# Kernel tuning notes

Measured on AMD Instinct MI355X. Metric: run time of the kernel, lower is better.

The kernel has to match this reference:

```python
import jax, jax.numpy as jnp
import numpy as np

V, E, H, HC = 20000, 300, 512, 256
B, N, LE, NW, LW, NC, LC = 16, 64, 16, 8, 16, 64, 16


def _gru_dir(xg, W_hh, b_hh, reverse):
    # xg: [B, T, 3*Hc] precomputed input gates; returns final hidden [B, Hc]
    xs = jnp.swapaxes(xg, 0, 1)
    if reverse:
        xs = xs[::-1]
    h0 = jnp.zeros((xg.shape[0], W_hh.shape[1]), xg.dtype)

    def step(h, xt):
        hr, hz, hn = jnp.split(h @ W_hh.T + b_hh, 3, axis=-1)
        xr, xz, xn = jnp.split(xt, 3, axis=-1)
        r = jax.nn.sigmoid(xr + hr)
        z = jax.nn.sigmoid(xz + hz)
        n = jnp.tanh(xn + r * hn)
        return (1.0 - z) * n + z * h, None

    hT, _ = jax.lax.scan(step, h0, xs)
    return hT


def _bigru(x, Wif, Whf, bif, bhf, Wib, Whb, bib, bhb):
    # x: [B, T, D] -> concat(fwd final, bwd final) = [B, 2*Hc]  (matches torch h_n.permute(1,0,2).reshape)
    hf = _gru_dir(x @ Wif.T + bif, Whf, bhf, False)
    hb = _gru_dir(x @ Wib.T + bib, Whb, bhb, True)
    return jnp.concatenate([hf, hb], axis=-1)


def setup_inputs() -> dict:
    key = jax.random.key(0)
    ks = iter(jax.random.split(key, 64))
    f = lambda *s: jax.random.normal(next(ks), s, jnp.float32) * 0.05
    ri = lambda *s: jax.random.randint(next(ks), s, 0, V)
    return {
        "emb_table": f(V, E),
        "W_prj": f(H, E),
        "dn_Wif": f(3 * HC, H), "dn_Whf": f(3 * HC, HC), "dn_bif": f(3 * HC), "dn_bhf": f(3 * HC),
        "dn_Wib": f(3 * HC, H), "dn_Whb": f(3 * HC, HC), "dn_bib": f(3 * HC), "dn_bhb": f(3 * HC),
        "W_e": f(H, H), "W_l": f(H, H), "W_w": f(H, H),
        "Wg": f(H, H), "bg": f(H),
        "diff_Wif": f(3 * H, H), "diff_Whf": f(3 * H, H), "diff_bif": f(3 * H), "diff_bhf": f(3 * H),
        "diff_Wib": f(3 * H, H), "diff_Whb": f(3 * H, H), "diff_bib": f(3 * H), "diff_bhb": f(3 * H),
        "Wc": f(1, 2 * H), "bc": f(1),
        "Wa1": f(2 * H, 2 * H), "ba1": f(2 * H), "Wa2": f(1, 2 * H), "ba2": f(1),
        "local_adj": jnp.zeros((64, 64), jnp.float32),
        "obs": ri(B, 32),
        "local_graph": ri(64, 8),
        "entities": ri(B, N, LE),
        "locals_": ri(B, N, LE),
        "worlds": ri(B, N, NW, LW),
        "commands": ri(B, NC, LC),
    }


def reference(emb_table, W_prj,
              dn_Wif, dn_Whf, dn_bif, dn_bhf, dn_Wib, dn_Whb, dn_bib, dn_bhb,
              W_e, W_l, W_w, Wg, bg,
              diff_Wif, diff_Whf, diff_bif, diff_bhf, diff_Wib, diff_Whb, diff_bib, diff_bhb,
              Wc, bc, Wa1, ba1, Wa2, ba2,
              local_adj, obs, local_graph, entities, locals_, worlds, commands):
    dn = (dn_Wif, dn_Whf, dn_bif, dn_bhf, dn_Wib, dn_Whb, dn_bib, dn_bhb)
    emb = lambda ids: emb_table[ids] @ W_prj.T  # embedding lookup + no-bias projection to H

    b, n, le = entities.shape
    ent_h = _bigru(emb(entities).reshape(b * n, le, H), *dn).reshape(b, n, H)
    ll = locals_.shape[-1]
    loc_h = _bigru(emb(locals_).reshape(b * n, ll, H), *dn).reshape(b, n, H)
    nw, lw = worlds.shape[2], worlds.shape[3]
    w_h = _bigru(emb(worlds).reshape(b * n * nw, lw, H), *dn).reshape(b, n, nw, H)
    worlds_sum = (w_h @ W_w).sum(axis=2)  # [b, n, H]

    # torch.ones(H,H) + W_e  ==  broadcastable 1.0 + W_e
    graph_hidden = jax.nn.elu(ent_h @ (1.0 + W_e)) + jax.nn.elu(loc_h @ W_l) + worlds_sum
    graph_encoding = jax.nn.elu(jax.nn.elu(graph_hidden) @ Wg.T + bg)  # graph_prj (dropout=eval identity)

    # value network: 'diff' path
    diff_h = _bigru(graph_encoding, diff_Wif, diff_Whf, diff_bif, diff_bhf,
                    diff_Wib, diff_Whb, diff_bib, diff_bhb)  # [b, 2H]
    value = (diff_h @ Wc.T + bc).reshape(b, 1, 1)

    nc, lc = commands.shape[1], commands.shape[2]
    c_h = _bigru(emb(commands).reshape(b * nc, lc, H), *dn).reshape(b, nc, H)

    rep = jnp.concatenate([
        jnp.broadcast_to(c_h[:, None, :, :], (b, n, nc, H)),
        jnp.broadcast_to(graph_encoding[:, :, None, :], (b, n, nc, H)),
    ], axis=-1)  # [b, n, nc, 2H]
    s = jax.nn.elu(rep @ Wa1.T + ba1) @ Wa2.T + ba2  # att_cmd (dropout p=0)
    scores = s[..., 0].mean(axis=1)  # mean over entities -> [b, nc]

    mask = commands.sum(axis=2) > 0
    probs = jax.nn.softmax(jnp.where(mask, scores, -1e9), axis=1)
    index = jnp.argmax(probs, axis=1).reshape(1, b, 1)  # deterministic stand-in for multinomial(1)
    return scores, index, value
```

## Files before the change

### kernel.cpp

```cpp
#include <hip/hip_runtime.h>
#include <stdint.h>

#define DEVFN __device__ __forceinline__

typedef __attribute__((ext_vector_type(4))) float fx4;
typedef __attribute__((ext_vector_type(8))) short sx8;
typedef __bf16 bf16x8 __attribute__((ext_vector_type(8)));

DEVFN float eluf(float x){ return x>0.f ? x : __expf(x)-1.f; }
DEVFN float sigm(float x){ return 1.f/(1.f+__expf(-x)); }
DEVFN float tanhf_(float x){ float cx=fminf(10.f,fmaxf(-10.f,x)); float e=__expf(-2.f*cx); return (1.f-e)/(1.f+e); }

DEVFN fx4 MFMA(sx8 a, sx8 b, fx4 c){
  return __builtin_amdgcn_mfma_f32_16x16x32_bf16(
      __builtin_bit_cast(bf16x8,a), __builtin_bit_cast(bf16x8,b), c, 0,0,0);
}
DEVFN void splitf(float x, short& hi, short& lo){
  __bf16 h = (__bf16)x; hi = __builtin_bit_cast(short, h);
  __bf16 l = (__bf16)(x - (float)h); lo = __builtin_bit_cast(short, l);
}

struct TT { const float* src; float* dst; int srows, scols, drows; };
struct TTs { TT t[4]; };
__global__ void k_prep_t(TTs ts){
  TT tk = ts.t[blockIdx.y];
  size_t tot = (size_t)tk.drows * tk.srows;
  for (size_t i = (size_t)blockIdx.x*256 + threadIdx.x; i < tot; i += (size_t)gridDim.x*256){
    int c = (int)(i / tk.srows), r = (int)(i % tk.srows);
    tk.dst[i] = (c < tk.scols) ? tk.src[(size_t)r*tk.scols + c] : 0.f;
  }
}
struct PL { const float* src; __bf16* hi; __bf16* lo; size_t n; };
struct PLs { PL t[2]; };
__global__ void k_prep_planes(PLs ts){
  PL tk = ts.t[blockIdx.y];
  for (size_t i = (size_t)blockIdx.x*256 + threadIdx.x; i < tk.n; i += (size_t)gridDim.x*256){
    float x = tk.src[i];
    __bf16 h = (__bf16)x;
    tk.hi[i] = h; tk.lo[i] = (__bf16)(x - (float)h);
  }
}
struct BC { const float* src; __bf16* dst; size_t n; };
struct BCs { BC t[2]; };
__global__ void k_prep_b16(BCs ts){
  BC tk = ts.t[blockIdx.y];
  for (size_t i = (size_t)blockIdx.x*256 + threadIdx.x; i < tk.n; i += (size_t)gridDim.x*256)
    tk.dst[i] = (__bf16)tk.src[i];
}
__global__ void k_toks(const int* __restrict__ ents, const int* __restrict__ locs,
                       const int* __restrict__ wrl, const int* __restrict__ cmd,
                       int* __restrict__ toks){
  int idx = blockIdx.x*256 + threadIdx.x;
  if (idx >= 2*16*11264) return;
  int dir = idx / (16*11264);
  int rem = idx % (16*11264);
  int s = rem / 11264, c = rem % 11264;
  const int* tp;
  if (c<1024) tp = ents + c*16;
  else if (c<2048) tp = locs + (c-1024)*16;
  else if (c<10240) tp = wrl + (c-2048)*16;
  else tp = cmd + (c-10240)*16;
  toks[idx] = tp[dir ? 15-s : s];
}
__global__ void k_cat_bias(const float* __restrict__ a, const float* __restrict__ b,
                           float* __restrict__ o){
  int i = blockIdx.x*256 + threadIdx.x;
  if (i < 768) o[i] = a[i];
  else if (i < 1536) o[i] = b[i-768];
}

template<int EPI, int OBF>
__global__ __launch_bounds__(256) void gemm_k(
    const float* __restrict__ A, const float* __restrict__ B,
    const float* __restrict__ bias, void* __restrict__ out,
    int M, int N, int Kpad, int Kreal, int lda, int ldb)
{
  int bm = blockIdx.y*64, bn = blockIdx.x*64;
  int tid = threadIdx.x, l = tid&63, w = tid>>6;
  int wm = (w>>1)*32, wn = (w&1)*32;
  int lr = l&15, lk = l>>4;
  fx4 acc[2][2] = {};
  for (int k0 = 0; k0 < Kpad; k0 += 32) {
    sx8 ahi[2], alo[2], bhi[2], blo[2];
    bool full = (k0 + 32 <= Kreal);
    #pragma unroll
    for (int i=0;i<2;i++){
      int row = bm + wm + i*16 + lr; row = row < M ? row : M-1;
      int col = bn + wn + i*16 + lr;
      const float* ap = A + (size_t)row*lda + k0 + lk*8;
      const float* bp = B + (size_t)col*ldb + k0 + lk*8;
      float av[8], bv[8];
      if (full){
        *(fx4*)av = *(const fx4*)ap; *(fx4*)(av+4) = *(const fx4*)(ap+4);
        *(fx4*)bv = *(const fx4*)bp; *(fx4*)(bv+4) = *(const fx4*)(bp+4);
      } else {
        #pragma unroll
        for (int j=0;j<8;j++){
          int k = k0 + lk*8 + j;
          av[j] = (k < Kreal) ? ap[j] : 0.f;
          bv[j] = (k < Kreal) ? bp[j] : 0.f;
        }
      }
      #pragma unroll
      for (int j=0;j<8;j++){
        short h,lo2; splitf(av[j], h, lo2); ahi[i][j]=h; alo[i][j]=lo2;
        splitf(bv[j], h, lo2); bhi[i][j]=h; blo[i][j]=lo2;
      }
    }
    #pragma unroll
    for (int i=0;i<2;i++)
      #pragma unroll
      for (int j=0;j<2;j++){
        acc[i][j] = MFMA(alo[i], bhi[j], acc[i][j]);
        acc[i][j] = MFMA(ahi[i], blo[j], acc[i][j]);
        acc[i][j] = MFMA(ahi[i], bhi[j], acc[i][j]);
      }
  }
  #pragma unroll
  for (int i=0;i<2;i++)
    #pragma unroll
    for (int j=0;j<2;j++)
      #pragma unroll
      for (int q=0;q<4;q++){
        int m = bm + wm + i*16 + lk*4 + q;
        int n = bn + wn + j*16 + lr;
        if (m < M){
          float v = acc[i][j][q];
          if (EPI>=1) v += bias[n];
          if (EPI==2) v = eluf(v);
          if (OBF) ((__bf16*)out)[(size_t)m*N + n] = (__bf16)v;
          else     ((float*)out)[(size_t)m*N + n] = v;
        }
      }
}

__global__ __launch_bounds__(256) void dn_step(
  const __bf16* __restrict__ Hshi, const __bf16* __restrict__ Hslo,
  __bf16* __restrict__ Hdhi, __bf16* __restrict__ Hdlo,
  const __bf16* __restrict__ Whi, const __bf16* __restrict__ Wlo,
  const float* __restrict__ bias, const float* __restrict__ T, int tstride,
  const int* __restrict__ toks,
  float* __restrict__ seqh, int s, int dir)
{
  int bm = blockIdx.x*64;
  int bj = blockIdx.y*64;
  int tid = threadIdx.x, l = tid&63, w = tid>>6;
  int wm = (w>>1)*32, wn = (w&1)*32;
  int lr = l&15, lk = l>>4;
  fx4 acc[2][2][3] = {};
  if (s > 0){
    for (int kk=0;kk<8;kk++){
      sx8 ah[2], al[2];
      #pragma unroll
      for (int i=0;i<2;i++){
        int m = bm + wm + i*16 + lr;
        ah[i] = *(const sx8*)(Hshi + (size_t)m*256 + kk*32 + lk*8);
        al[i] = *(const sx8*)(Hslo + (size_t)m*256 + kk*32 + lk*8);
      }
      #pragma unroll
      for (int jt=0;jt<2;jt++){
        #pragma unroll
        for (int role=0;role<3;role++){
          int col = role*256 + bj + wn + jt*16 + lr;
          sx8 bhf = *(const sx8*)(Whi + (size_t)col*256 + kk*32 + lk*8);
          sx8 blf = *(const sx8*)(Wlo + (size_t)col*256 + kk*32 + lk*8);
          #pragma unroll
          for (int i=0;i<2;i++){
            fx4 a = acc[i][jt][role];
            a = MFMA(al[i], bhf, a);
            a = MFMA(ah[i], blf, a);
            a = MFMA(ah[i], bhf, a);
            acc[i][jt][role] = a;
          }
        }
      }
    }
  }
  const int* tks = toks + s*11264;
  #pragma unroll
  for (int i=0;i<2;i++){
    #pragma unroll
    for (int q=0;q<4;q++){
      int m = bm + wm + i*16 + lk*4 + q;
      int tok = tks[m];
      const float* trow = T + (size_t)tok*tstride;
      #pragma unroll
      for (int jt=0;jt<2;jt++){
        int j = bj + wn + jt*16 + lr;
        float hr = acc[i][jt][0][q] + bias[j];
        float hz = acc[i][jt][1][q] + bias[256+j];
        float hn = acc[i][jt][2][q] + bias[512+j];
        float xr = trow[j], xz = trow[256+j], xn = trow[512+j];
        float ho = 0.f;
        if (s > 0) ho = (float)Hshi[(size_t)m*256+j] + (float)Hslo[(size_t)m*256+j];
        float r = sigm(xr+hr), z = sigm(xz+hz);
        float n = tanhf_(xn + r*hn);
        float v = (1.f-z)*n + z*ho;
        __bf16 hh = (__bf16)v;
        Hdhi[(size_t)m*256+j] = hh;
        Hdlo[(size_t)m*256+j] = (__bf16)(v - (float)hh);
        if (s == 15) seqh[(size_t)m*512 + dir*256 + j] = v;
      }
    }
  }
}

__global__ void k_wsum(const float* __restrict__ seqh, float* __restrict__ ws){
  int r = blockIdx.x;
  for (int c = threadIdx.x; c < 512; c += 256){
    float a = 0.f;
    #pragma unroll
    for (int w8=0; w8<8; w8++) a += seqh[((size_t)2048 + r*8 + w8)*512 + c];
    ws[(size_t)r*512 + c] = a;
  }
}
__global__ void k_rowsum(const float* __restrict__ seqh, float* __restrict__ rs){
  int r = blockIdx.x, l = threadIdx.x;
  float a = 0.f;
  for (int c=l;c<512;c+=64) a += seqh[(size_t)r*512+c];
  #pragma unroll
  for (int o=32;o>0;o>>=1) a += __shfl_down(a,o);
  if (l==0) rs[r]=a;
}
__global__ void k_combine(const float* __restrict__ E1, const float* __restrict__ E2,
                          const float* __restrict__ E3, const float* __restrict__ rs,
                          float* __restrict__ y){
  size_t i = (size_t)blockIdx.x*256 + threadIdx.x;
  int r = (int)(i >> 9);
  float g = eluf(E1[i] + rs[r]) + eluf(E2[i]) + E3[i];
  y[i] = eluf(g);
}

__global__ __launch_bounds__(256) void diff_step(
  const float* __restrict__ hsrc, float* __restrict__ hdst,
  const __bf16* __restrict__ Whf, const __bf16* __restrict__ Whb,
  const float* __restrict__ bhf, const float* __restrict__ bhb,
  const __bf16* __restrict__ Xf, const __bf16* __restrict__ Xb, int t)
{
  int wg = blockIdx.x;
  int dir = wg>>3, seg = wg&7;
  const __bf16* W = dir? Whb: Whf;
  const float* bh = dir? bhb: bhf;
  const __bf16* X = dir? Xb: Xf;
  int tt = dir? 63-t : t;
  int tid = threadIdx.x, l = tid&63, w = tid>>6;
  int lr=l&15, lk=l>>4;
  int jbase = seg*64 + w*16;
  fx4 acc[3] = {};
  const float* hrow = hsrc + (size_t)dir*16*512;
  for (int kk=0;kk<16;kk++){
    const float* ap = hrow + (size_t)lr*512 + kk*32 + lk*8;
    float av[8];
    *(fx4*)av = *(const fx4*)ap; *(fx4*)(av+4) = *(const fx4*)(ap+4);
    sx8 ah, al;
    #pragma unroll
    for (int j=0;j<8;j++){ short h,lo; splitf(av[j],h,lo); ah[j]=h; al[j]=lo; }
    #pragma unroll
    for (int role=0;role<3;role++){
      int col = role*512 + jbase + lr;
      sx8 b = *(const sx8*)(W + (size_t)col*512 + kk*32 + lk*8);
      acc[role] = MFMA(al, b, acc[role]);
      acc[role] = MFMA(ah, b, acc[role]);
    }
  }
  #pragma unroll
  for (int q=0;q<4;q++){
    int m = lk*4+q;
    int j = jbase + lr;
    float hr = acc[0][q] + bh[j];
    float hz = acc[1][q] + bh[512+j];
    float hn = acc[2][q] + bh[1024+j];
    const __bf16* xrow = X + ((size_t)m*64 + tt)*1536;
    float xr = (float)xrow[j], xz = (float)xrow[512+j], xn = (float)xrow[1024+j];
    float ho = hrow[(size_t)m*512 + j];
    float r = sigm(xr+hr), z = sigm(xz+hz);
    float n = tanhf_(xn + r*hn);
    hdst[((size_t)dir*16 + m)*512 + j] = (1.f-z)*n + z*ho;
  }
}

__global__ __launch_bounds__(256) void k_score(
  const float* __restrict__ Amat, const float* __restrict__ Gmat,
  const float* __restrict__ Wa2, const float* __restrict__ ba2, float* __restrict__ sc)
{
  __shared__ float red[4];
  int p = blockIdx.x, b = p>>6, tid = threadIdx.x;
  float av[4], wv[4];
  #pragma unroll
  for (int k=0;k<4;k++){ av[k] = Amat[(size_t)p*1024 + tid + k*256]; wv[k] = Wa2[tid + k*256]; }
  float acc = 0.f;
  for (int n=0;n<64;n++){
    const float* g = Gmat + ((size_t)b*64+n)*1024;
    #pragma unroll
    for (int k=0;k<4;k++) acc += wv[k]*eluf(av[k] + g[tid + k*256]);
  }
  #pragma unroll
  for (int o=32;o>0;o>>=1) acc += __shfl_down(acc,o);
  if ((tid&63)==0) red[tid>>6] = acc;
  __syncthreads();
  if (tid==0) sc[p] = (red[0]+red[1]+red[2]+red[3])*(1.f/64.f) + ba2[0];
}

__global__ void k_final(const float* __restrict__ sc, const int* __restrict__ cmds,
                        const float* __restrict__ hfin, const float* __restrict__ Wc,
                        const float* __restrict__ bc, float* __restrict__ out)
{
  int b = blockIdx.x, l = threadIdx.x;
  out[b*64+l] = sc[b*64+l];
  int ssum = 0;
  const int* cr = cmds + (b*64+l)*16;
  #pragma unroll
  for (int k=0;k<16;k++) ssum += cr[k];
  float v = ssum>0 ? sc[b*64+l] : -1e9f;
  int idx = l;
  #pragma unroll
  for (int o=32;o>0;o>>=1){
    float ov = __shfl_down(v,o); int oi = __shfl_down(idx,o);
    if (ov > v || (ov==v && oi<idx)) { v=ov; idx=oi; }
  }
  if (l==0) out[1024 + b] = (float)idx;
  float a = 0.f;
  for (int j=l;j<512;j+=64) a += hfin[(size_t)b*512+j] * Wc[j];
  for (int j=l;j<512;j+=64) a += hfin[(size_t)(16+b)*512+j] * Wc[512+j];
  #pragma unroll
  for (int o=32;o>0;o>>=1) a += __shfl_down(a,o);
  if (l==0) out[1040 + b] = a + bc[0];
}

static inline void launch_gemm(hipStream_t st, const float* A, const float* B,
                               const float* bias, void* out, int M, int N,
                               int Kpad, int Kreal, int lda, int ldb, int epi, int obf)
{
  dim3 g(N/64, (M+63)/64), blk(256);
  if      (epi==0 && obf==0) gemm_k<0,0><<<g,blk,0,st>>>(A,B,bias,out,M,N,Kpad,Kreal,lda,ldb);
  else if (epi==1 && obf==0) gemm_k<1,0><<<g,blk,0,st>>>(A,B,bias,out,M,N,Kpad,Kreal,lda,ldb);
  else if (epi==2 && obf==0) gemm_k<2,0><<<g,blk,0,st>>>(A,B,bias,out,M,N,Kpad,Kreal,lda,ldb);
  else                       gemm_k<1,1><<<g,blk,0,st>>>(A,B,bias,out,M,N,Kpad,Kreal,lda,ldb);
}

extern "C" void kernel_launch(void* const* d_in, const int* in_sizes, int n_in,
                              void* d_out, int out_size, void* d_ws, size_t ws_size,
                              hipStream_t stream) {
  (void)in_sizes; (void)n_in; (void)out_size;
  const float* emb   = (const float*)d_in[0];
  const float* W_prj = (const float*)d_in[1];
  const float* dnWif = (const float*)d_in[2];
  const float* dnWhf = (const float*)d_in[3];
  const float* dnbif = (const float*)d_in[4];
  const float* dnbhf = (const float*)d_in[5];
  const float* dnWib = (const float*)d_in[6];
  const float* dnWhb = (const float*)d_in[7];
  const float* dnbib = (const float*)d_in[8];
  const float* dnbhb = (const float*)d_in[9];
  const float* W_e   = (const float*)d_in[10];
  const float* W_l   = (const float*)d_in[11];
  const float* W_w   = (const float*)d_in[12];
  const float* Wg    = (const float*)d_in[13];
  const float* bg    = (const float*)d_in[14];
  const float* dWif  = (const float*)d_in[15];
  const float* dWhf  = (const float*)d_in[16];
  const float* dbif  = (const float*)d_in[17];
  const float* dbhf  = (const float*)d_in[18];
  const float* dWib  = (const float*)d_in[19];
  const float* dWhb  = (const float*)d_in[20];
  const float* dbib  = (const float*)d_in[21];
  const float* dbhb  = (const float*)d_in[22];
  const float* Wc    = (const float*)d_in[23];
  const float* bc    = (const float*)d_in[24];
  const float* Wa1   = (const float*)d_in[25];
  const float* ba1   = (const float*)d_in[26];
  const float* Wa2   = (const float*)d_in[27];
  const float* ba2   = (const float*)d_in[28];
  const int* ents = (const int*)d_in[32];
  const int* locs = (const int*)d_in[33];
  const int* wrl  = (const int*)d_in[34];
  const int* cmds = (const int*)d_in[35];

  char* ws = (char*)d_ws;
  size_t off = 0;
#define WSP(name, type, count) type* name = (type*)(ws + off); off += (((size_t)(count))*sizeof(type) + 255) & ~(size_t)255;
  WSP(pWprjT, float, 320*512);
  WSP(pC2,    float, 1536*320);
  WSP(pB2,    float, 1536);
  WSP(pWhFhi, __bf16, 768*256);
  WSP(pWhFlo, __bf16, 768*256);
  WSP(pWhBhi, __bf16, 768*256);
  WSP(pWhBlo, __bf16, 768*256);
  WSP(pWeT,   float, 512*512);
  WSP(pWlT,   float, 512*512);
  WSP(pWwT,   float, 512*512);
  WSP(pdWhF,  __bf16, 1536*512);
  WSP(pdWhB,  __bf16, 1536*512);
  WSP(pSeqh,  float, 11264*512);
  WSP(pH0hi,  __bf16, 11264*256);
  WSP(pH0lo,  __bf16, 11264*256);
  WSP(pH1hi,  __bf16, 11264*256);
  WSP(pH1lo,  __bf16, 11264*256);
  WSP(pToks,  int,    2*16*11264);
  WSP(pHA,    float, 32*512);
  WSP(pHB,    float, 32*512);
  WSP(pRs,    float, 1024);
  WSP(pScf,   float, 1024);
#undef WSP
  float* pT = (float*)(ws + off);
  size_t trem = (ws_size > off) ? (ws_size - off) : 0;
  bool comb = trem >= (size_t)20000*1536*sizeof(float);

  const size_t SZ = (size_t)1024*512*4;
  char* sc = (char*)pT;
  float* pWsum = (float*)(sc + 0*SZ);
  float* pE1   = (float*)(sc + 1*SZ);
  float* pE2   = (float*)(sc + 2*SZ);
  float* pE3   = (float*)(sc + 3*SZ);
  float* pY    = (float*)(sc + 4*SZ);
  float* pGe   = (float*)(sc + 5*SZ);
  float* pAmat = (float*)(sc + 6*SZ);
  float* pGmat = (float*)(sc + 8*SZ);
  __bf16* pXf  = (__bf16*)(sc + 10*SZ);
  __bf16* pXb  = (__bf16*)(sc + 10*SZ + (size_t)1024*1536*2);

  TTs tt;
  tt.t[0] = { W_prj, pWprjT, 512, 300, 320 };
  tt.t[1] = { W_e,   pWeT,   512, 512, 512 };
  tt.t[2] = { W_l,   pWlT,   512, 512, 512 };
  tt.t[3] = { W_w,   pWwT,   512, 512, 512 };
  k_prep_t<<<dim3(256,4), 256, 0, stream>>>(tt);
  PLs pl;
  pl.t[0] = { dnWhf, pWhFhi, pWhFlo, (size_t)768*256 };
  pl.t[1] = { dnWhb, pWhBhi, pWhBlo, (size_t)768*256 };
  k_prep_planes<<<dim3(256,2), 256, 0, stream>>>(pl);
  BCs bcs;
  bcs.t[0] = { dWhf, pdWhF, (size_t)1536*512 };
  bcs.t[1] = { dWhb, pdWhB, (size_t)1536*512 };
  k_prep_b16<<<dim3(512,2), 256, 0, stream>>>(bcs);
  k_toks<<<1408, 256, 0, stream>>>(ents, locs, wrl, cmds, pToks);
  k_cat_bias<<<6, 256, 0, stream>>>(dnbif, dnbib, pB2);

  launch_gemm(stream, dnWif, pWprjT, nullptr, pC2,           768, 320, 512, 512, 512, 512, 0, 0);
  launch_gemm(stream, dnWib, pWprjT, nullptr, pC2 + 768*320, 768, 320, 512, 512, 512, 512, 0, 0);

  if (comb){
    launch_gemm(stream, emb, pC2, pB2, pT, 20000, 1536, 320, 300, 300, 320, 1, 0);
    for (int dir = 0; dir < 2; ++dir){
      const __bf16* Whi = dir? pWhBhi : pWhFhi;
      const __bf16* Wlo = dir? pWhBlo : pWhFlo;
      const float*  bh  = dir? dnbhb  : dnbhf;
      const int*    tks = pToks + (size_t)dir*16*11264;
      const float*  Td  = pT + dir*768;
      for (int s = 0; s < 16; ++s){
        __bf16 *shi, *slo, *dhi, *dlo;
        if ((s & 1) == 0){ shi=pH0hi; slo=pH0lo; dhi=pH1hi; dlo=pH1lo; }
        else             { shi=pH1hi; slo=pH1lo; dhi=pH0hi; dlo=pH0lo; }
        dn_step<<<dim3(176,4), 256, 0, stream>>>(shi, slo, dhi, dlo,
            Whi, Wlo, bh, Td, 1536, tks, pSeqh, s, dir);
      }
    }
  } else {
    for (int dir = 0; dir < 2; ++dir){
      launch_gemm(stream, emb, dir? pC2 + 768*320 : pC2, dir? dnbib : dnbif, pT,
                  20000, 768, 320, 300, 300, 320, 1, 0);
      const __bf16* Whi = dir? pWhBhi : pWhFhi;
      const __bf16* Wlo = dir? pWhBlo : pWhFlo;
      const float*  bh  = dir? dnbhb  : dnbhf;
      const int*    tks = pToks + (size_t)dir*16*11264;
      for (int s = 0; s < 16; ++s){
        __bf16 *shi, *slo, *dhi, *dlo;
        if ((s & 1) == 0){ shi=pH0hi; slo=pH0lo; dhi=pH1hi; dlo=pH1lo; }
        else             { shi=pH1hi; slo=pH1lo; dhi=pH0hi; dlo=pH0lo; }
        dn_step<<<dim3(176,4), 256, 0, stream>>>(shi, slo, dhi, dlo,
            Whi, Wlo, bh, pT, 768, tks, pSeqh, s, dir);
      }
    }
  }

  k_wsum<<<1024, 256, 0, stream>>>(pSeqh, pWsum);
  k_rowsum<<<1024, 64, 0, stream>>>(pSeqh, pRs);
  launch_gemm(stream, pSeqh,                   pWeT, nullptr, pE1, 1024, 512, 512, 512, 512, 512, 0, 0);
  launch_gemm(stream, pSeqh + (size_t)1024*512,pWlT, nullptr, pE2, 1024, 512, 512, 512, 512, 512, 0, 0);
  launch_gemm(stream, pWsum,                   pWwT, nullptr, pE3, 1024, 512, 512, 512, 512, 512, 0, 0);
  k_combine<<<2048, 256, 0, stream>>>(pE1, pE2, pE3, pRs, pY);
  launch_gemm(stream, pY, Wg, bg, pGe, 1024, 512, 512, 512, 512, 512, 2, 0);
  launch_gemm(stream, pGe, dWif, dbif, pXf, 1024, 1536, 512, 512, 512, 512, 1, 1);
  launch_gemm(stream, pGe, dWib, dbib, pXb, 1024, 1536, 512, 512, 512, 512, 1, 1);
  launch_gemm(stream, pSeqh + (size_t)10240*512, Wa1, nullptr, pAmat, 1024, 1024, 512, 512, 512, 1024, 0, 0);
  launch_gemm(stream, pGe, Wa1 + 512, ba1, pGmat, 1024, 1024, 512, 512, 512, 1024, 1, 0);
  k_score<<<1024, 256, 0, stream>>>(pAmat, pGmat, Wa2, ba2, pScf);
  hipMemsetAsync(pHA, 0, 32*512*sizeof(float), stream);
  float* ha = pHA; float* hb = pHB;
  for (int t=0; t<64; ++t){
    diff_step<<<16, 256, 0, stream>>>(ha, hb, pdWhF, pdWhB, dbhf, dbhb, pXf, pXb, t);
    float* tmp = ha; ha = hb; hb = tmp;
  }
  k_final<<<16, 64, 0, stream>>>(pScf, cmds, ha, Wc, bc, (float*)d_out);
}
```

Measured before the change: 2.862 ms.

## Run forward and backward GRU directions in one launch with smaller row tiles

The dn_step kernel now takes two direction descriptors and picks one per block, so forward and backward recurrences run together in 16 launches instead of 32. Each block now covers 32 rows instead of 64, which quadruples the grid (704x4 blocks) and raises occupancy per launch. Two extra hidden-state buffers are placed after the gate table so the directions do not clash. The cost is that weight fragments are reused across fewer rows, so each block does more global weight loads per MFMA, and the new path needs extra workspace.

```diff
diff --git a/kernel.cpp b/kernel.cpp
--- a/kernel.cpp
+++ b/kernel.cpp
@@ -134,73 +134,71 @@
       }
 }
 
-__global__ __launch_bounds__(256) void dn_step(
-  const __bf16* __restrict__ Hshi, const __bf16* __restrict__ Hslo,
-  __bf16* __restrict__ Hdhi, __bf16* __restrict__ Hdlo,
-  const __bf16* __restrict__ Whi, const __bf16* __restrict__ Wlo,
-  const float* __restrict__ bias, const float* __restrict__ T, int tstride,
-  const int* __restrict__ toks,
-  float* __restrict__ seqh, int s, int dir)
+struct DnDir {
+  const __bf16 *Hshi, *Hslo;
+  __bf16 *Hdhi, *Hdlo;
+  const __bf16 *Whi, *Wlo;
+  const float *bias;
+  const float *T;
+  const int *toks;
+  int tstride;
+  int dircol;
+};
+__global__ __launch_bounds__(256) void dn_step(DnDir d0, DnDir d1,
+                                               float* __restrict__ seqh, int s)
 {
-  int bm = blockIdx.x*64;
+  int bx = blockIdx.x;
+  int sel = (bx >= 352) ? 1 : 0;
+  DnDir d = sel ? d1 : d0;
+  int bm = (bx - sel*352)*32;
   int bj = blockIdx.y*64;
   int tid = threadIdx.x, l = tid&63, w = tid>>6;
-  int wm = (w>>1)*32, wn = (w&1)*32;
+  int wm = (w&1)*16, wn = (w>>1)*32;
   int lr = l&15, lk = l>>4;
-  fx4 acc[2][2][3] = {};
+  fx4 acc[2][3] = {};
   if (s > 0){
     for (int kk=0;kk<8;kk++){
-      sx8 ah[2], al[2];
-      #pragma unroll
-      for (int i=0;i<2;i++){
-        int m = bm + wm + i*16 + lr;
-        ah[i] = *(const sx8*)(Hshi + (size_t)m*256 + kk*32 + lk*8);
-        al[i] = *(const sx8*)(Hslo + (size_t)m*256 + kk*32 + lk*8);
-      }
+      int m = bm + wm + lr;
+      sx8 ah = *(const sx8*)(d.Hshi + (size_t)m*256 + kk*32 + lk*8);
+      sx8 al = *(const sx8*)(d.Hslo + (size_t)m*256 + kk*32 + lk*8);
       #pragma unroll
       for (int jt=0;jt<2;jt++){
         #pragma unroll
         for (int role=0;role<3;role++){
           int col = role*256 + bj + wn + jt*16 + lr;
-          sx8 bhf = *(const sx8*)(Whi + (size_t)col*256 + kk*32 + lk*8);
-          sx8 blf = *(const sx8*)(Wlo + (size_t)col*256 + kk*32 + lk*8);
-          #pragma unroll
-          for (int i=0;i<2;i++){
-            fx4 a = acc[i][jt][role];
-            a = MFMA(al[i], bhf, a);
-            a = MFMA(ah[i], blf, a);
-            a = MFMA(ah[i], bhf, a);
-            acc[i][jt][role] = a;
-          }
+          sx8 bhf = *(const sx8*)(d.Whi + (size_t)col*256 + kk*32 + lk*8);
+          sx8 blf = *(const sx8*)(d.Wlo + (size_t)col*256 + kk*32 + lk*8);
+          fx4 a = acc[jt][role];
+          a = MFMA(al, bhf, a);
+          a = MFMA(ah, blf, a);
+          a = MFMA(ah, bhf, a);
+          acc[jt][role] = a;
         }
       }
     }
   }
-  const int* tks = toks + s*11264;
-  #pragma unroll
-  for (int i=0;i<2;i++){
-    #pragma unroll
-    for (int q=0;q<4;q++){
-      int m = bm + wm + i*16 + lk*4 + q;
-      int tok = tks[m];
-      const float* trow = T + (size_t)tok*tstride;
-      #pragma unroll
-      for (int jt=0;jt<2;jt++){
-        int j = bj + wn + jt*16 + lr;
-        float hr = acc[i][jt][0][q] + bias[j];
-        float hz = acc[i][jt][1][q] + bias[256+j];
-        float hn = acc[i][jt][2][q] + bias[512+j];
-        float xr = trow[j], xz = trow[256+j], xn = trow[512+j];
-        float ho = 0.f;
-        if (s > 0) ho = (float)Hshi[(size_t)m*256+j] + (float)Hslo[(size_t)m*256+j];
-        float r = sigm(xr+hr), z = sigm(xz+hz);
-        float n = tanhf_(xn + r*hn);
-        float v = (1.f-z)*n + z*ho;
-        __bf16 hh = (__bf16)v;
-        Hdhi[(size_t)m*256+j] = hh;
-        Hdlo[(size_t)m*256+j] = (__bf16)(v - (float)hh);
-        if (s == 15) seqh[(size_t)m*512 + dir*256 + j] = v;
-      }
+  const int* tks = d.toks + s*11264;
+  #pragma unroll
+  for (int q=0;q<4;q++){
+    int m = bm + wm + lk*4 + q;
+    int tok = tks[m];
+    const float* trow = d.T + (size_t)tok*d.tstride;
+    #pragma unroll
+    for (int jt=0;jt<2;jt++){
+      int j = bj + wn + jt*16 + lr;
+      float hr = acc[jt][0][q] + d.bias[j];
+      float hz = acc[jt][1][q] + d.bias[256+j];
+      float hn = acc[jt][2][q] + d.bias[512+j];
+      float xr = trow[j], xz = trow[256+j], xn = trow[512+j];
+      float ho = 0.f;
+      if (s > 0) ho = (float)d.Hshi[(size_t)m*256+j] + (float)d.Hslo[(size_t)m*256+j];
+      float r = sigm(xr+hr), z = sigm(xz+hz);
+      float n = tanhf_(xn + r*hn);
+      float v = (1.f-z)*n + z*ho;
+      __bf16 hh = (__bf16)v;
+      d.Hdhi[(size_t)m*256+j] = hh;
+      d.Hdlo[(size_t)m*256+j] = (__bf16)(v - (float)hh);
+      if (s == 15) seqh[(size_t)m*512 + d.dircol*256 + j] = v;
     }
   }
 }
@@ -404,7 +402,13 @@
 #undef WSP
   float* pT = (float*)(ws + off);
   size_t trem = (ws_size > off) ? (ws_size - off) : 0;
-  bool comb = trem >= (size_t)20000*1536*sizeof(float);
+  const size_t TBL = (size_t)20000*1536*sizeof(float);
+  const size_t HB  = (size_t)11264*256*sizeof(__bf16);
+  bool comb = trem >= TBL;
+  bool conc = trem >= TBL + 4*HB;
+  char* h2 = (char*)pT + TBL;
+  __bf16* pH2hi[2] = { (__bf16*)h2,            (__bf16*)(h2 + 2*HB) };
+  __bf16* pH2lo[2] = { (__bf16*)(h2 + HB),     (__bf16*)(h2 + 3*HB) };
 
   const size_t SZ = (size_t)1024*512*4;
   char* sc = (char*)pT;
@@ -439,36 +443,40 @@
   launch_gemm(stream, dnWif, pWprjT, nullptr, pC2,           768, 320, 512, 512, 512, 512, 0, 0);
   launch_gemm(stream, dnWib, pWprjT, nullptr, pC2 + 768*320, 768, 320, 512, 512, 512, 512, 0, 0);
 
-  if (comb){
+  if (comb && conc){
+    launch_gemm(stream, emb, pC2, pB2, pT, 20000, 1536, 320, 300, 300, 320, 1, 0);
+    for (int s = 0; s < 16; ++s){
+      int pp = s & 1;
+      DnDir D0 = { pp? pH1hi:pH0hi, pp? pH1lo:pH0lo,
+                   pp? pH0hi:pH1hi, pp? pH0lo:pH1lo,
+                   pWhFhi, pWhFlo, dnbhf, pT,        pToks,                1536, 0 };
+      DnDir D1 = { pH2hi[pp], pH2lo[pp], pH2hi[pp^1], pH2lo[pp^1],
+                   pWhBhi, pWhBlo, dnbhb, pT + 768,  pToks + 16*11264,     1536, 1 };
+      dn_step<<<dim3(704,4), 256, 0, stream>>>(D0, D1, pSeqh, s);
+    }
+  } else if (comb){
     launch_gemm(stream, emb, pC2, pB2, pT, 20000, 1536, 320, 300, 300, 320, 1, 0);
     for (int dir = 0; dir < 2; ++dir){
-      const __bf16* Whi = dir? pWhBhi : pWhFhi;
-      const __bf16* Wlo = dir? pWhBlo : pWhFlo;
-      const float*  bh  = dir? dnbhb  : dnbhf;
-      const int*    tks = pToks + (size_t)dir*16*11264;
-      const float*  Td  = pT + dir*768;
       for (int s = 0; s < 16; ++s){
-        __bf16 *shi, *slo, *dhi, *dlo;
-        if ((s & 1) == 0){ shi=pH0hi; slo=pH0lo; dhi=pH1hi; dlo=pH1lo; }
-        else             { shi=pH1hi; slo=pH1lo; dhi=pH0hi; dlo=pH0lo; }
-        dn_step<<<dim3(176,4), 256, 0, stream>>>(shi, slo, dhi, dlo,
-            Whi, Wlo, bh, Td, 1536, tks, pSeqh, s, dir);
+        int pp = s & 1;
+        DnDir D = { pp? pH1hi:pH0hi, pp? pH1lo:pH0lo,
+                    pp? pH0hi:pH1hi, pp? pH0lo:pH1lo,
+                    dir? pWhBhi:pWhFhi, dir? pWhBlo:pWhFlo, dir? dnbhb:dnbhf,
+                    pT + dir*768, pToks + (size_t)dir*16*11264, 1536, dir };
+        dn_step<<<dim3(352,4), 256, 0, stream>>>(D, D, pSeqh, s);
       }
     }
   } else {
     for (int dir = 0; dir < 2; ++dir){
       launch_gemm(stream, emb, dir? pC2 + 768*320 : pC2, dir? dnbib : dnbif, pT,
                   20000, 768, 320, 300, 300, 320, 1, 0);
-      const __bf16* Whi = dir? pWhBhi : pWhFhi;
-      const __bf16* Wlo = dir? pWhBlo : pWhFlo;
-      const float*  bh  = dir? dnbhb  : dnbhf;
-      const int*    tks = pToks + (size_t)dir*16*11264;
       for (int s = 0; s < 16; ++s){
-        __bf16 *shi, *slo, *dhi, *dlo;
-        if ((s & 1) == 0){ shi=pH0hi; slo=pH0lo; dhi=pH1hi; dlo=pH1lo; }
-        else             { shi=pH1hi; slo=pH1lo; dhi=pH0hi; dlo=pH0lo; }
-        dn_step<<<dim3(176,4), 256, 0, stream>>>(shi, slo, dhi, dlo,
-            Whi, Wlo, bh, pT, 768, tks, pSeqh, s, dir);
+        int pp = s & 1;
+        DnDir D = { pp? pH1hi:pH0hi, pp? pH1lo:pH0lo,
+                    pp? pH0hi:pH1hi, pp? pH0lo:pH1lo,
+                    dir? pWhBhi:pWhFhi, dir? pWhBlo:pWhFlo, dir? dnbhb:dnbhf,
+                    pT, pToks + (size_t)dir*16*11264, 768, dir };
+        dn_step<<<dim3(352,4), 256, 0, stream>>>(D, D, pSeqh, s);
       }
     }
   }
```

After: 3.585 ms. +25.3%, slower.
